# Performance work log

Hardware: AMD Instinct MI355X
Metric: run time of the kernel (lower is better)

The kernel has to match this reference:

```python
import jax, jax.numpy as jnp
import numpy as np

ROW, COL, KSIZE = 7, 7, 5   # unfold_row, unfold_column, kernel_size
EPS = 1e-5


def _unfold(x, row, col):
    # non-overlapping nn.Unfold(kernel=(row,col), stride=(row,col)) -> [B*L, C, row, col]
    B, C, H, W = x.shape
    nr, nc = H // row, W // col
    return x.reshape(B, C, nr, row, nc, col).transpose(0, 2, 4, 1, 3, 5).reshape(B * nr * nc, C, row, col)


def _fold(x, B, H, W):
    BL, C, row, col = x.shape
    nr, nc = H // row, W // col
    return x.reshape(B, nr, nc, C, row, col).transpose(0, 3, 1, 4, 2, 5).reshape(B, C, H, W)


def _bilinear_shift(img, yq, xq):
    # out[n,i,j] = img[n, yq[n,i], xq[n,j]] with bilinear interp, zeros outside
    # (matches F.grid_sample(align_corners=True, padding_mode='zeros') for pure translations)
    N, H, W = img.shape
    y0 = jnp.floor(yq); x0 = jnp.floor(xq)
    fy = yq - y0; fx = xq - x0
    y0 = y0.astype(jnp.int32); x0 = x0.astype(jnp.int32)
    out = jnp.zeros_like(img)
    for dy, wy in ((0, 1.0 - fy), (1, fy)):
        yi = y0 + dy
        vy = wy * ((yi >= 0) & (yi < H)).astype(img.dtype)                              # [N,H]
        rows = jnp.take_along_axis(img, jnp.clip(yi, 0, H - 1)[:, :, None], axis=1)     # [N,H,W]
        for dx, wx in ((0, 1.0 - fx), (1, fx)):
            xi = x0 + dx
            vx = wx * ((xi >= 0) & (xi < W)).astype(img.dtype)                          # [N,W]
            vals = jnp.take_along_axis(rows, jnp.clip(xi, 0, W - 1)[:, None, :], axis=2)
            out = out + vy[:, :, None] * vx[:, None, :] * vals
    return out


def setup_inputs():
    key = jax.random.key(0)
    k1, k2, k3 = jax.random.split(key, 3)
    feat = jax.random.normal(k1, (16, 8, 126, 126), jnp.float32)
    # encoder logits are class probabilities over the 100 Gaussian prototypes
    logits = jax.nn.softmax(jax.random.normal(k2, (16, 100, 126, 126), jnp.float32), axis=1)
    s = jnp.linspace(0.2, 3.0, 10)
    sx, sy = jnp.meshgrid(s, s, indexing='ij')            # matches torch.meshgrid init
    sigma_x = sx.reshape(-1)
    sigma_y = sy.reshape(-1)
    opacity = jax.nn.sigmoid(jnp.ones((100,), jnp.float32))
    rho = jax.random.uniform(k3, (100,), jnp.float32, -0.5, 0.5)
    return {"feat": feat, "logits": logits, "sigma_x": sigma_x,
            "sigma_y": sigma_y, "opacity": opacity, "rho": rho}


def reference(feat, logits, sigma_x, sigma_y, opacity, rho):
    B, C, H, W = feat.shape
    # H, W are multiples of ROW/COL so the bicubic resize to the ceil-multiple size is identity
    uf = _unfold(feat, ROW, COL)        # [BL, C, 7, 7]
    ul = _unfold(logits, ROW, COL)      # [BL, 100, 7, 7]
    BL = uf.shape[0]
    N = ROW * COL                        # 49 points per patch
    # weighted_gaussian_parameters: contract over class dim, then mean over batch(=B*L)
    lg = ul.transpose(0, 2, 3, 1)        # [BL, 7, 7, 100]
    wsx = (lg * sigma_x).sum(-1).reshape(BL, N).mean(0)   # [N]
    wsy = (lg * sigma_y).sum(-1).reshape(BL, N).mean(0)
    wop = (lg * opacity).sum(-1).reshape(BL, N).mean(0)
    wrho = (lg * rho).sum(-1).reshape(BL, N).mean(0)
    # 2x2 covariance per point; analytic inverse / det
    a = wsx * wsx + EPS
    d = wsy * wsy + EPS
    b = wrho * wsx * wsy
    det = a * d - b * b                                    # [N], > 0
    ax = jnp.linspace(-5.0, 5.0, KSIZE)
    gx, gy = jnp.meshgrid(ax, ax, indexing='ij')           # [K,K]
    z = -0.5 * (d[:, None, None] * gx**2 - 2.0 * b[:, None, None] * gx * gy
                + a[:, None, None] * gy**2) / det[:, None, None]
    kern = jnp.exp(z) / (2.0 * jnp.pi * jnp.sqrt(det)[:, None, None])
    kern = kern / kern.max(axis=(-2, -1), keepdims=True)   # [N,K,K], max-normalized
    # pad kernel up to the patch raster size
    ph, pw = ROW - KSIZE, COL - KSIZE
    kern = jnp.pad(kern, ((0, 0), (ph // 2, ph - ph // 2), (pw // 2, pw - pw // 2)))
    # translate kernel p to its point location (affine_grid/grid_sample semantics)
    ii, jj = jnp.meshgrid(jnp.arange(ROW), jnp.arange(COL), indexing='ij')
    yp = ii.reshape(-1).astype(kern.dtype)                 # p = y*COL + x (generate_meshgrid order)
    xp = jj.reshape(-1).astype(kern.dtype)
    tx = (1.0 - 2.0 * xp / ROW) * (COL - 1) / 2.0          # divisor ROW mirrors original (ROW==COL)
    ty = (1.0 - 2.0 * yp / COL) * (ROW - 1) / 2.0
    xq = jnp.arange(COL, dtype=kern.dtype)[None, :] + tx[:, None]   # [N,COL]
    yq = jnp.arange(ROW, dtype=kern.dtype)[None, :] + ty[:, None]   # [N,ROW]
    kt = _bilinear_shift(kern, yq, xq)                     # [N,7,7]
    # colors at each point are the patch pixel values (fetching_features_from_tensor)
    colors = uf.reshape(BL, C, N).transpose(0, 2, 1)       # [BL,N,C]
    # splat: sum_p color[bl,p,c] * opacity_w[p] * kernel_p(i,j)  (fused, avoids [BL,N,C,7,7])
    out = jnp.einsum('lpc,p,pij->lcij', colors, wop, kt)
    return _fold(out, B, H, W)
```

## Files before the change

kernel.cpp:

```cpp
#include <hip/hip_runtime.h>

#define W 126
#define NPIX 15876
#define NB 16
#define NCH 8
#define NCLS 100

#define CC 10
#define NYCH 10
#define NPAIR 63
#define NWID (NYCH * NB * NPAIR)
#define NBLK_A (NWID / 4)

#define WS_ACC_OFF 0
#define WS_MT_OFF 256
#define WS_PART_OFF 4096

__global__ __launch_bounds__(256) void ga_reduce(
    const float* __restrict__ logits,
    const float* __restrict__ sx, const float* __restrict__ sy,
    const float* __restrict__ op, const float* __restrict__ rho,
    float* __restrict__ part) {
  __shared__ float s_data[4][64][17];
  __shared__ float s_bin[196];
  __shared__ int   s_m[4];
  const int t    = threadIdx.x;
  const int w    = t >> 6;
  const int lane = t & 63;

  for (int i = t; i < 196; i += 256) s_bin[i] = 0.f;

  const int wid  = blockIdx.x * 4 + w;
  const int cy   = wid / (NB * NPAIR);
  int rem = wid - cy * (NB * NPAIR);
  const int b    = rem / NPAIR;
  const int pair = rem - b * NPAIR;
  const int m    = (2 * pair) % 7;
  if (lane == 0) s_m[w] = m;

  float a[4][4];
#pragma unroll
  for (int k = 0; k < 4; ++k)
#pragma unroll
    for (int e = 0; e < 4; ++e) a[k][e] = 0.f;

  if (lane < 63) {
    const int c0 = cy * CC;
    const float4* base = reinterpret_cast<const float4*>(
        logits + ((size_t)b * NCLS + c0) * NPIX + (size_t)pair * 252) + lane;

    float4 v[CC];
#pragma unroll
    for (int cc = 0; cc < CC; ++cc) v[cc] = base[(size_t)cc * (NPIX / 4)];

#pragma unroll
    for (int cc = 0; cc < CC; ++cc) {
      const int c = c0 + cc;
      const float4 vv = v[cc];
      const float p0 = sx[c], p1 = sy[c], p2 = op[c], p3 = rho[c];
      a[0][0] += vv.x * p0; a[0][1] += vv.y * p0; a[0][2] += vv.z * p0; a[0][3] += vv.w * p0;
      a[1][0] += vv.x * p1; a[1][1] += vv.y * p1; a[1][2] += vv.z * p1; a[1][3] += vv.w * p1;
      a[2][0] += vv.x * p2; a[2][1] += vv.y * p2; a[2][2] += vv.z * p2; a[2][3] += vv.w * p2;
      a[3][0] += vv.x * p3; a[3][1] += vv.y * p3; a[3][2] += vv.z * p3; a[3][3] += vv.w * p3;
    }
  }

#pragma unroll
  for (int k = 0; k < 4; ++k) {
    s_data[w][lane][k * 4 + 0] = a[k][0];
    s_data[w][lane][k * 4 + 1] = a[k][1];
    s_data[w][lane][k * 4 + 2] = a[k][2];
    s_data[w][lane][k * 4 + 3] = a[k][3];
  }
  __syncthreads();

  if (t < 224) {
    const int ww  = t / 56;
    const int r56 = t - ww * 56;
    const int k   = r56 / 14;
    const int rr  = r56 - k * 14;
    const int rs  = rr / 7;
    const int n   = rr - rs * 7;
    float s = 0.f;
#pragma unroll
    for (int j = 0; j < 18; ++j) {
      const int f = rs * 126 + n + 7 * j;
      s += s_data[ww][f >> 2][k * 4 + (f & 3)];
    }
    const int mrow = (s_m[ww] + rs) % 7;
    atomicAdd(&s_bin[k * 49 + mrow * 7 + n], s);
  }
  __syncthreads();

  float* my = part + (size_t)blockIdx.x * 196;
  for (int i = t; i < 196; i += 256) my[i] = s_bin[i];
}

__global__ __launch_bounds__(256) void ga_final(const float* __restrict__ part,
                                                float* __restrict__ acc) {
  __shared__ float4 red[256];
  const int h = blockIdx.x;
  const int t = threadIdx.x;
  float4 s = make_float4(0.f, 0.f, 0.f, 0.f);
  for (int j = t; j < NBLK_A; j += 256) {
    const float4 v =
        *reinterpret_cast<const float4*>(part + (size_t)j * 196 + h * 4);
    s.x += v.x; s.y += v.y; s.z += v.z; s.w += v.w;
  }
  red[t] = s;
  __syncthreads();
#pragma unroll
  for (int off = 128; off; off >>= 1) {
    if (t < off) {
      red[t].x += red[t + off].x; red[t].y += red[t + off].y;
      red[t].z += red[t + off].z; red[t].w += red[t + off].w;
    }
    __syncthreads();
  }
  if (t == 0) *reinterpret_cast<float4*>(acc + h * 4) = red[0];
}

__global__ __launch_bounds__(64) void gb_build(const float* __restrict__ acc,
                                               float* __restrict__ MT) {
  __shared__ float s_kern[49][49];
  const int p = threadIdx.x;
  for (int i = p; i < 49; i += 64) {
    MT[i * 52 + 49] = 0.f;
    MT[i * 52 + 50] = 0.f;
    MT[i * 52 + 51] = 0.f;
  }
  if (p < 49) {
    const float inv = 1.0f / 5184.0f;
    const float wsx = acc[p]        * inv;
    const float wsy = acc[49 + p]   * inv;
    const float wop = acc[98 + p]   * inv;
    const float wrh = acc[147 + p]  * inv;
    const float av = wsx * wsx + 1e-5f;
    const float dv = wsy * wsy + 1e-5f;
    const float bv = wrh * wsx * wsy;
    const float det = av * dv - bv * bv;
    const float norm = 1.0f / (6.283185307179586f * sqrtf(det));
    float tmp[5][5];
    float mx = 0.f;
#pragma unroll
    for (int i = 0; i < 5; ++i) {
      const float gx = -5.0f + 2.5f * (float)i;
#pragma unroll
      for (int j = 0; j < 5; ++j) {
        const float gy = -5.0f + 2.5f * (float)j;
        const float z = -0.5f * (dv*gx*gx - 2.0f*bv*gx*gy + av*gy*gy) / det;
        const float v = expf(z) * norm;
        tmp[i][j] = v;
        mx = fmaxf(mx, v);
      }
    }
    const float rmx = 1.0f / mx;
#pragma unroll
    for (int i = 0; i < 49; ++i) s_kern[p][i] = 0.f;
#pragma unroll
    for (int i = 0; i < 5; ++i)
#pragma unroll
      for (int j = 0; j < 5; ++j)
        s_kern[p][(i + 1) * 7 + (j + 1)] = tmp[i][j] * rmx;

    const int yp = p / 7, xp = p % 7;
    const float tx = (1.0f - (2.0f * (float)xp) / 7.0f) * 3.0f;
    const float ty = (1.0f - (2.0f * (float)yp) / 7.0f) * 3.0f;
    for (int i = 0; i < 7; ++i) {
      const float yq  = (float)i + ty;
      const float y0f = floorf(yq);
      const float fy  = yq - y0f;
      const int   y0  = (int)y0f;
      for (int j = 0; j < 7; ++j) {
        const float xq  = (float)j + tx;
        const float x0f = floorf(xq);
        const float fx  = xq - x0f;
        const int   x0  = (int)x0f;
        float v = 0.f;
        for (int dy = 0; dy < 2; ++dy) {
          const int yi = y0 + dy;
          if (yi < 0 || yi > 6) continue;
          const float wy = dy ? fy : (1.0f - fy);
          for (int dx = 0; dx < 2; ++dx) {
            const int xi = x0 + dx;
            if (xi < 0 || xi > 6) continue;
            const float wx = dx ? fx : (1.0f - fx);
            v += wy * wx * s_kern[p][yi * 7 + xi];
          }
        }
        MT[(i * 7 + j) * 52 + p] = wop * v;
      }
    }
  }
}

__global__ __launch_bounds__(256) void gc_splat(
    const float* __restrict__ feat, const float* __restrict__ MT,
    float* __restrict__ out) {
  __shared__ __align__(16) float s_mt[49 * 52];
  __shared__ __align__(16) float s_fp[18 * 52];
  const int t = threadIdx.x;
  for (int i = t; i < 49 * 52; i += 256) s_mt[i] = MT[i];
  const int blk   = blockIdx.x;
  const int plane = blk / 18;
  const int pr    = blk - plane * 18;
  const float* src = feat + (size_t)plane * NPIX + (size_t)pr * 7 * W;
  for (int i = t; i < 882; i += 256) {
    const int py = i / W;
    const int xx = i - py * W;
    const int pc = xx / 7;
    const int px = xx - pc * 7;
    s_fp[pc * 52 + py * 7 + px] = src[i];
  }
  __syncthreads();
  float* dst = out + (size_t)plane * NPIX + (size_t)pr * 7 * W;
  for (int i = t; i < 882; i += 256) {
    const int yy = i / W;
    const int xx = i - yy * W;
    const int pc = xx / 7;
    const int q  = yy * 7 + (xx - pc * 7);
    const float4* mv = reinterpret_cast<const float4*>(s_mt + q * 52);
    const float4* fv = reinterpret_cast<const float4*>(s_fp + pc * 52);
    float s = 0.f;
#pragma unroll
    for (int r = 0; r < 12; ++r) {
      const float4 mm = mv[r];
      const float4 ff = fv[r];
      s += ff.x * mm.x + ff.y * mm.y + ff.z * mm.z + ff.w * mm.w;
    }
    s += s_fp[pc * 52 + 48] * s_mt[q * 52 + 48];
    dst[i] = s;
  }
}

extern "C" void kernel_launch(void* const* d_in, const int* in_sizes, int n_in,
                              void* d_out, int out_size, void* d_ws, size_t ws_size,
                              hipStream_t stream) {
  const float* feat   = (const float*)d_in[0];
  const float* logits = (const float*)d_in[1];
  const float* sx     = (const float*)d_in[2];
  const float* sy     = (const float*)d_in[3];
  const float* op     = (const float*)d_in[4];
  const float* rho    = (const float*)d_in[5];
  float* outp = (float*)d_out;
  float* ws   = (float*)d_ws;
  float* acc  = ws + WS_ACC_OFF;
  float* MT   = ws + WS_MT_OFF;
  float* part = ws + WS_PART_OFF;

  ga_reduce<<<NBLK_A, 256, 0, stream>>>(logits, sx, sy, op, rho, part);
  ga_final<<<49, 256, 0, stream>>>(part, acc);
  gb_build<<<1, 64, 0, stream>>>(acc, MT);
  gc_splat<<<NB * NCH * 18, 256, 0, stream>>>(feat, MT, outp);
}
```

Measured before the change: 62.47 us.

## Register-tile splat kernel: each thread computes a 2x7 output block

The splat kernel now handles two patch-rows per block with 128 threads. Each thread computes 14 outputs (two patches by seven columns of one row) in registers, so every feature vector and kernel-matrix float4 loaded from shared memory is reused across several outputs instead of being re-read for each pixel. The matrix copy into shared memory is vectorised and the padding lanes are zeroed so a 13-step float4 loop replaces the scalar tail. This should cut LDS traffic per output. In exchange it uses fewer blocks and threads, and each thread writes 14 consecutive floats, which coalesces less well than the old one-pixel-per-thread stores.

```diff
diff --git a/kernel.cpp b/kernel.cpp
--- a/kernel.cpp
+++ b/kernel.cpp
@@ -194,42 +194,68 @@
   }
 }
 
-__global__ __launch_bounds__(256) void gc_splat(
+__global__ __launch_bounds__(128) void gc_splat(
     const float* __restrict__ feat, const float* __restrict__ MT,
     float* __restrict__ out) {
   __shared__ __align__(16) float s_mt[49 * 52];
-  __shared__ __align__(16) float s_fp[18 * 52];
+  __shared__ __align__(16) float s_fp[36 * 52];
   const int t = threadIdx.x;
-  for (int i = t; i < 49 * 52; i += 256) s_mt[i] = MT[i];
-  const int blk   = blockIdx.x;
-  const int plane = blk / 18;
-  const int pr    = blk - plane * 18;
-  const float* src = feat + (size_t)plane * NPIX + (size_t)pr * 7 * W;
-  for (int i = t; i < 882; i += 256) {
-    const int py = i / W;
-    const int xx = i - py * W;
-    const int pc = xx / 7;
-    const int px = xx - pc * 7;
-    s_fp[pc * 52 + py * 7 + px] = src[i];
-  }
-  __syncthreads();
-  float* dst = out + (size_t)plane * NPIX + (size_t)pr * 7 * W;
-  for (int i = t; i < 882; i += 256) {
-    const int yy = i / W;
-    const int xx = i - yy * W;
-    const int pc = xx / 7;
-    const int q  = yy * 7 + (xx - pc * 7);
-    const float4* mv = reinterpret_cast<const float4*>(s_mt + q * 52);
-    const float4* fv = reinterpret_cast<const float4*>(s_fp + pc * 52);
-    float s = 0.f;
-#pragma unroll
-    for (int r = 0; r < 12; ++r) {
-      const float4 mm = mv[r];
-      const float4 ff = fv[r];
-      s += ff.x * mm.x + ff.y * mm.y + ff.z * mm.z + ff.w * mm.w;
-    }
-    s += s_fp[pc * 52 + 48] * s_mt[q * 52 + 48];
-    dst[i] = s;
+  {
+    const float4* s4 = reinterpret_cast<const float4*>(MT);
+    float4* d4 = reinterpret_cast<float4*>(s_mt);
+    for (int i = t; i < (49 * 52) / 4; i += 128) d4[i] = s4[i];
+  }
+  for (int i = t; i < 36 * 3; i += 128) {
+    const int pt = i / 3;
+    s_fp[pt * 52 + 49 + (i - pt * 3)] = 0.f;
+  }
+  const int plane = blockIdx.x / 9;
+  const int bsg   = blockIdx.x - plane * 9;
+  const float* src = feat + (size_t)plane * NPIX + (size_t)bsg * (14 * W);
+  for (int i = t; i < 14 * W; i += 128) {
+    const int y  = i / W;
+    const int x  = i - y * W;
+    const int s  = y / 7, py = y - s * 7;
+    const int pc = x / 7, px = x - pc * 7;
+    s_fp[(s * 18 + pc) * 52 + py * 7 + px] = src[i];
+  }
+  __syncthreads();
+
+  if (t < 126) {
+    const int s   = t / 63;
+    const int r63 = t - s * 63;
+    const int g   = r63 / 7;
+    const int yy  = r63 - g * 7;
+    const float* frow0 = s_fp + (s * 18 + 2 * g) * 52;
+    const float* frow1 = frow0 + 52;
+    const float* mrow  = s_mt + (yy * 7) * 52;
+
+    float acc[2][7];
+#pragma unroll
+    for (int j = 0; j < 2; ++j)
+#pragma unroll
+      for (int xx = 0; xx < 7; ++xx) acc[j][xx] = 0.f;
+
+#pragma unroll
+    for (int r = 0; r < 13; ++r) {
+      const float4 f0 = *reinterpret_cast<const float4*>(frow0 + 4 * r);
+      const float4 f1 = *reinterpret_cast<const float4*>(frow1 + 4 * r);
+#pragma unroll
+      for (int xx = 0; xx < 7; ++xx) {
+        const float4 mv =
+            *reinterpret_cast<const float4*>(mrow + xx * 52 + 4 * r);
+        acc[0][xx] += f0.x * mv.x + f0.y * mv.y + f0.z * mv.z + f0.w * mv.w;
+        acc[1][xx] += f1.x * mv.x + f1.y * mv.y + f1.z * mv.z + f1.w * mv.w;
+      }
+    }
+
+    float* dst = out + (size_t)plane * NPIX +
+                 (size_t)((2 * bsg + s) * 7 + yy) * W + 14 * g;
+#pragma unroll
+    for (int j = 0; j < 2; ++j)
+#pragma unroll
+      for (int xx = 0; xx < 7; ++xx)
+        dst[j * 7 + xx] = acc[j][xx];
   }
 }
 
@@ -251,5 +277,5 @@
   ga_reduce<<<NBLK_A, 256, 0, stream>>>(logits, sx, sy, op, rho, part);
   ga_final<<<49, 256, 0, stream>>>(part, acc);
   gb_build<<<1, 64, 0, stream>>>(acc, MT);
-  gc_splat<<<NB * NCH * 18, 256, 0, stream>>>(feat, MT, outp);
-}
+  gc_splat<<<128 * 9, 128, 0, stream>>>(feat, MT, outp);
+}
```

Result: slower. 73.91 us (+18.3%).

## Fuse final reduction and kernel build into ga_reduce via last-block ticket

Applied to the files above, without the earlier changes.

Removes the separate ga_final and gb_build launches. The last block to finish ga_reduce, detected with an atomic ticket counter, now sums the per-block partials and builds the MT matrix. Each wave also handles three row-pairs instead of one, cutting the block count from 2520 to 840, so there are fewer partials to reduce. In exchange, the final reduction runs serially in one block, with 196 threads each doing 840 loads, and a memset is needed to reset the counter on every call.

```diff
diff --git a/kernel.cpp b/kernel.cpp
--- a/kernel.cpp
+++ b/kernel.cpp
@@ -7,35 +7,36 @@
 #define NCLS 100
 
 #define CC 10
-#define NYCH 10
-#define NPAIR 63
-#define NWID (NYCH * NB * NPAIR)
-#define NBLK_A (NWID / 4)
-
-#define WS_ACC_OFF 0
+#define NBLK_A 840
+
 #define WS_MT_OFF 256
+#define WS_CNT_OFF 3072
 #define WS_PART_OFF 4096
 
 __global__ __launch_bounds__(256) void ga_reduce(
     const float* __restrict__ logits,
     const float* __restrict__ sx, const float* __restrict__ sy,
     const float* __restrict__ op, const float* __restrict__ rho,
-    float* __restrict__ part) {
+    float* __restrict__ part, float* __restrict__ MT, int* __restrict__ cnt) {
   __shared__ float s_data[4][64][17];
   __shared__ float s_bin[196];
+  __shared__ float s_acc[196];
   __shared__ int   s_m[4];
+  __shared__ int   s_ticket;
   const int t    = threadIdx.x;
   const int w    = t >> 6;
   const int lane = t & 63;
 
   for (int i = t; i < 196; i += 256) s_bin[i] = 0.f;
 
-  const int wid  = blockIdx.x * 4 + w;
-  const int cy   = wid / (NB * NPAIR);
-  int rem = wid - cy * (NB * NPAIR);
-  const int b    = rem / NPAIR;
-  const int pair = rem - b * NPAIR;
-  const int m    = (2 * pair) % 7;
+  const int wid = blockIdx.x * 4 + w;
+  const int cy  = wid / 336;
+  int rem = wid - cy * 336;
+  const int b   = rem / 21;
+  rem -= b * 21;
+  const int m   = rem / 3;
+  const int kg  = rem - m * 3;
+  const int pbase = (4 * m) % 7;
   if (lane == 0) s_m[w] = m;
 
   float a[4][4];
@@ -46,22 +47,25 @@
 
   if (lane < 63) {
     const int c0 = cy * CC;
-    const float4* base = reinterpret_cast<const float4*>(
-        logits + ((size_t)b * NCLS + c0) * NPIX + (size_t)pair * 252) + lane;
-
-    float4 v[CC];
-#pragma unroll
-    for (int cc = 0; cc < CC; ++cc) v[cc] = base[(size_t)cc * (NPIX / 4)];
-
-#pragma unroll
-    for (int cc = 0; cc < CC; ++cc) {
-      const int c = c0 + cc;
-      const float4 vv = v[cc];
-      const float p0 = sx[c], p1 = sy[c], p2 = op[c], p3 = rho[c];
-      a[0][0] += vv.x * p0; a[0][1] += vv.y * p0; a[0][2] += vv.z * p0; a[0][3] += vv.w * p0;
-      a[1][0] += vv.x * p1; a[1][1] += vv.y * p1; a[1][2] += vv.z * p1; a[1][3] += vv.w * p1;
-      a[2][0] += vv.x * p2; a[2][1] += vv.y * p2; a[2][2] += vv.z * p2; a[2][3] += vv.w * p2;
-      a[3][0] += vv.x * p3; a[3][1] += vv.y * p3; a[3][2] += vv.z * p3; a[3][3] += vv.w * p3;
+    const float* img = logits + ((size_t)b * NCLS + c0) * NPIX;
+#pragma unroll
+    for (int r = 0; r < 3; ++r) {
+      const int pair = pbase + 7 * (kg * 3 + r);
+      const float4* base =
+          reinterpret_cast<const float4*>(img + (size_t)pair * 252) + lane;
+      float4 v[CC];
+#pragma unroll
+      for (int cc = 0; cc < CC; ++cc) v[cc] = base[(size_t)cc * (NPIX / 4)];
+#pragma unroll
+      for (int cc = 0; cc < CC; ++cc) {
+        const int c = c0 + cc;
+        const float4 vv = v[cc];
+        const float p0 = sx[c], p1 = sy[c], p2 = op[c], p3 = rho[c];
+        a[0][0] += vv.x * p0; a[0][1] += vv.y * p0; a[0][2] += vv.z * p0; a[0][3] += vv.w * p0;
+        a[1][0] += vv.x * p1; a[1][1] += vv.y * p1; a[1][2] += vv.z * p1; a[1][3] += vv.w * p1;
+        a[2][0] += vv.x * p2; a[2][1] += vv.y * p2; a[2][2] += vv.z * p2; a[2][3] += vv.w * p2;
+        a[3][0] += vv.x * p3; a[3][1] += vv.y * p3; a[3][2] += vv.z * p3; a[3][3] += vv.w * p3;
+      }
     }
   }
 
@@ -94,101 +98,97 @@
 
   float* my = part + (size_t)blockIdx.x * 196;
   for (int i = t; i < 196; i += 256) my[i] = s_bin[i];
-}
-
-__global__ __launch_bounds__(256) void ga_final(const float* __restrict__ part,
-                                                float* __restrict__ acc) {
-  __shared__ float4 red[256];
-  const int h = blockIdx.x;
-  const int t = threadIdx.x;
-  float4 s = make_float4(0.f, 0.f, 0.f, 0.f);
-  for (int j = t; j < NBLK_A; j += 256) {
-    const float4 v =
-        *reinterpret_cast<const float4*>(part + (size_t)j * 196 + h * 4);
-    s.x += v.x; s.y += v.y; s.z += v.z; s.w += v.w;
-  }
-  red[t] = s;
-  __syncthreads();
-#pragma unroll
-  for (int off = 128; off; off >>= 1) {
-    if (t < off) {
-      red[t].x += red[t + off].x; red[t].y += red[t + off].y;
-      red[t].z += red[t + off].z; red[t].w += red[t + off].w;
-    }
-    __syncthreads();
-  }
-  if (t == 0) *reinterpret_cast<float4*>(acc + h * 4) = red[0];
-}
-
-__global__ __launch_bounds__(64) void gb_build(const float* __restrict__ acc,
-                                               float* __restrict__ MT) {
-  __shared__ float s_kern[49][49];
-  const int p = threadIdx.x;
-  for (int i = p; i < 49; i += 64) {
-    MT[i * 52 + 49] = 0.f;
-    MT[i * 52 + 50] = 0.f;
-    MT[i * 52 + 51] = 0.f;
-  }
-  if (p < 49) {
-    const float inv = 1.0f / 5184.0f;
-    const float wsx = acc[p]        * inv;
-    const float wsy = acc[49 + p]   * inv;
-    const float wop = acc[98 + p]   * inv;
-    const float wrh = acc[147 + p]  * inv;
-    const float av = wsx * wsx + 1e-5f;
-    const float dv = wsy * wsy + 1e-5f;
-    const float bv = wrh * wsx * wsy;
-    const float det = av * dv - bv * bv;
-    const float norm = 1.0f / (6.283185307179586f * sqrtf(det));
-    float tmp[5][5];
-    float mx = 0.f;
-#pragma unroll
-    for (int i = 0; i < 5; ++i) {
-      const float gx = -5.0f + 2.5f * (float)i;
-#pragma unroll
-      for (int j = 0; j < 5; ++j) {
-        const float gy = -5.0f + 2.5f * (float)j;
-        const float z = -0.5f * (dv*gx*gx - 2.0f*bv*gx*gy + av*gy*gy) / det;
-        const float v = expf(z) * norm;
-        tmp[i][j] = v;
-        mx = fmaxf(mx, v);
+
+  __threadfence();
+  if (t == 0)
+    s_ticket = __hip_atomic_fetch_add(cnt, 1, __ATOMIC_ACQ_REL,
+                                      __HIP_MEMORY_SCOPE_AGENT);
+  __syncthreads();
+  if (s_ticket != NBLK_A - 1) return;
+
+  if (t < 196) {
+    float s0 = 0.f, s1 = 0.f, s2 = 0.f, s3 = 0.f;
+    for (int j = 0; j < NBLK_A; j += 4) {
+      s0 += part[(size_t)(j + 0) * 196 + t];
+      s1 += part[(size_t)(j + 1) * 196 + t];
+      s2 += part[(size_t)(j + 2) * 196 + t];
+      s3 += part[(size_t)(j + 3) * 196 + t];
+    }
+    s_acc[t] = (s0 + s1) + (s2 + s3);
+  }
+  __syncthreads();
+
+  if (t < 64) {
+    float (*s_kern)[49] = reinterpret_cast<float(*)[49]>(&s_data[0][0][0]);
+    const int p = t;
+    for (int i = p; i < 49; i += 64) {
+      MT[i * 52 + 49] = 0.f;
+      MT[i * 52 + 50] = 0.f;
+      MT[i * 52 + 51] = 0.f;
+    }
+    if (p < 49) {
+      const float inv = 1.0f / 5184.0f;
+      const float wsx = s_acc[p]        * inv;
+      const float wsy = s_acc[49 + p]   * inv;
+      const float wop = s_acc[98 + p]   * inv;
+      const float wrh = s_acc[147 + p]  * inv;
+      const float av = wsx * wsx + 1e-5f;
+      const float dv = wsy * wsy + 1e-5f;
+      const float bv = wrh * wsx * wsy;
+      const float det = av * dv - bv * bv;
+      const float norm = 1.0f / (6.283185307179586f * sqrtf(det));
+      float tmp[5][5];
+      float mx = 0.f;
+#pragma unroll
+      for (int i = 0; i < 5; ++i) {
+        const float gx = -5.0f + 2.5f * (float)i;
+#pragma unroll
+        for (int j = 0; j < 5; ++j) {
+          const float gy = -5.0f + 2.5f * (float)j;
+          const float z = -0.5f * (dv*gx*gx - 2.0f*bv*gx*gy + av*gy*gy) / det;
+          const float v = expf(z) * norm;
+          tmp[i][j] = v;
+          mx = fmaxf(mx, v);
+        }
       }
-    }
-    const float rmx = 1.0f / mx;
-#pragma unroll
-    for (int i = 0; i < 49; ++i) s_kern[p][i] = 0.f;
-#pragma unroll
-    for (int i = 0; i < 5; ++i)
-#pragma unroll
-      for (int j = 0; j < 5; ++j)
-        s_kern[p][(i + 1) * 7 + (j + 1)] = tmp[i][j] * rmx;
-
-    const int yp = p / 7, xp = p % 7;
-    const float tx = (1.0f - (2.0f * (float)xp) / 7.0f) * 3.0f;
-    const float ty = (1.0f - (2.0f * (float)yp) / 7.0f) * 3.0f;
-    for (int i = 0; i < 7; ++i) {
-      const float yq  = (float)i + ty;
-      const float y0f = floorf(yq);
-      const float fy  = yq - y0f;
-      const int   y0  = (int)y0f;
-      for (int j = 0; j < 7; ++j) {
-        const float xq  = (float)j + tx;
-        const float x0f = floorf(xq);
-        const float fx  = xq - x0f;
-        const int   x0  = (int)x0f;
-        float v = 0.f;
-        for (int dy = 0; dy < 2; ++dy) {
-          const int yi = y0 + dy;
-          if (yi < 0 || yi > 6) continue;
-          const float wy = dy ? fy : (1.0f - fy);
-          for (int dx = 0; dx < 2; ++dx) {
-            const int xi = x0 + dx;
-            if (xi < 0 || xi > 6) continue;
-            const float wx = dx ? fx : (1.0f - fx);
-            v += wy * wx * s_kern[p][yi * 7 + xi];
+      const float rmx = 1.0f / mx;
+#pragma unroll
+      for (int i = 0; i < 49; ++i) s_kern[p][i] = 0.f;
+#pragma unroll
+      for (int i = 0; i < 5; ++i)
+#pragma unroll
+        for (int j = 0; j < 5; ++j)
+          s_kern[p][(i + 1) * 7 + (j + 1)] = tmp[i][j] * rmx;
+
+      const int yp = p / 7, xp = p % 7;
+      const float tx = (1.0f - (2.0f * (float)xp) / 7.0f) * 3.0f;
+      const float ty = (1.0f - (2.0f * (float)yp) / 7.0f) * 3.0f;
+      for (int i = 0; i < 7; ++i) {
+        const float yq  = (float)i + ty;
+        const float y0f = floorf(yq);
+        const float fy  = yq - y0f;
+        const int   y0  = (int)y0f;
+        for (int j = 0; j < 7; ++j) {
+          const float xq  = (float)j + tx;
+          const float x0f = floorf(xq);
+          const float fx  = fy, dummy = 0.f;
+          (void)dummy;
+          const float fxr = xq - x0f;
+          const int   x0  = (int)x0f;
+          float v = 0.f;
+          for (int dy = 0; dy < 2; ++dy) {
+            const int yi = y0 + dy;
+            if (yi < 0 || yi > 6) continue;
+            const float wy = dy ? fy : (1.0f - fy);
+            for (int dx = 0; dx < 2; ++dx) {
+              const int xi = x0 + dx;
+              if (xi < 0 || xi > 6) continue;
+              const float wx = dx ? fxr : (1.0f - fxr);
+              v += wy * wx * s_kern[p][yi * 7 + xi];
+            }
           }
+          MT[(i * 7 + j) * 52 + p] = wop * v;
         }
-        MT[(i * 7 + j) * 52 + p] = wop * v;
       }
     }
   }
@@ -244,12 +244,12 @@
   const float* rho    = (const float*)d_in[5];
   float* outp = (float*)d_out;
   float* ws   = (float*)d_ws;
-  float* acc  = ws + WS_ACC_OFF;
-  float* MT   = ws + WS_MT_OFF;
-  float* part = ws + WS_PART_OFF;
-
-  ga_reduce<<<NBLK_A, 256, 0, stream>>>(logits, sx, sy, op, rho, part);
-  ga_final<<<49, 256, 0, stream>>>(part, acc);
-  gb_build<<<1, 64, 0, stream>>>(acc, MT);
-  gc_splat<<<NB * NCH * 18, 256, 0, stream>>>(feat, MT, outp);
+  float* MTp  = ws + WS_MT_OFF;
+  int*   cntp = (int*)(ws + WS_CNT_OFF);
+  float* partp = ws + WS_PART_OFF;
+
+  hipMemsetAsync(cntp, 0, 64, stream);
+  ga_reduce<<<NBLK_A, 256, 0, stream>>>(logits, sx, sy, op, rho,
+                                        partp, MTp, cntp);
+  gc_splat<<<NB * NCH * 18, 256, 0, stream>>>(feat, MTp, outp);
 }
```

Result: slower. 186.4 us (+198.3%).
